# Optimization experiments

Hardware: AMD Instinct MI355X
Metric: run time of the kernel (lower is better)

## Reference

```python
import jax, jax.numpy as jnp
import numpy as np

B, H, L, D = 2, 16, 2048, 64


def setup_inputs() -> dict:
    key = jax.random.key(0)
    ks = jax.random.split(key, 5)
    q = jax.random.normal(ks[0], (B, H, L, D), dtype=jnp.float32)
    k = jax.random.normal(ks[1], (B, H, L, D), dtype=jnp.float32)
    v = jax.random.normal(ks[2], (B, H, L, D), dtype=jnp.float32)
    pe_q = jax.random.normal(ks[3], (B, H, L, D), dtype=jnp.float32)
    pe_k = jax.random.normal(ks[4], (B, H, L, D), dtype=jnp.float32)
    # causal mask, broadcast over batch: True = keep
    mask = jnp.broadcast_to(jnp.tril(jnp.ones((L, L), dtype=bool)), (B, L, L))
    return {"q": q, "k": k, "v": v, "pe_q": pe_q, "pe_k": pe_k, "mask": mask}


def reference(q, k, v, pe_q, pe_k, mask):
    scale = q.shape[-1] ** (-0.5)
    # dual-score: content QK^T + positional PE_Q PE_K^T, fused before softmax
    attn = (jnp.einsum('bhqd,bhkd->bhqk', q, k)
            + jnp.einsum('bhqd,bhkd->bhqk', pe_q, pe_k)) * scale
    # mask: [B, L, L] -> [B, 1, L, L]; False positions get -inf
    attn = jnp.where(mask[:, None, :, :], attn, -jnp.inf)
    attn = jax.nn.softmax(attn, axis=-1)
    return jnp.einsum('bhqk,bhkd->bhqd', attn, v)
```

## Files before the change

### kernel.cpp

```cpp
#include <hip/hip_runtime.h>
#include <hip/hip_bf16.h>


typedef unsigned short u16;
typedef unsigned int   u32;
typedef __attribute__((ext_vector_type(8))) short bf16x8;
typedef __attribute__((ext_vector_type(4))) float f32x4;

#define L_SEQ 2048
#define D_DIM 64
#define BQ    64
#define BK    32
#define NQT   (L_SEQ / BQ)

__device__ __forceinline__ float bf2f(u32 lo16) {
    u32 u = lo16 << 16; float f; __builtin_memcpy(&f, &u, 4); return f;
}

__device__ __forceinline__ u32 pack_hi16(u32 lo_src, u32 hi_src) {
    return __builtin_amdgcn_perm(hi_src, lo_src, 0x07060302u);
}

__global__ void detect_dtype_kernel(const u16* __restrict__ q, int* __restrict__ flag) {
    const int lane = threadIdx.x;
    float x = fabsf(bf2f((u32)q[lane]));
    bool big = !(x <= 100.f);
    unsigned long long m = __ballot(big);
    if (lane == 0) *flag = (m != 0ull) ? 1 : 0;
}

__device__ __forceinline__ void split_pack(const float* x, uint4& h, uint4& l) {
    u32 xb[8], rb[8];
#pragma unroll
    for (int j = 0; j < 8; ++j) {
        __builtin_memcpy(&xb[j], &x[j], 4);
        u32 hb = xb[j] & 0xffff0000u;
        float hf; __builtin_memcpy(&hf, &hb, 4);
        float r = x[j] - hf;
        __builtin_memcpy(&rb[j], &r, 4);
    }
    h.x = pack_hi16(xb[0], xb[1]);
    h.y = pack_hi16(xb[2], xb[3]);
    h.z = pack_hi16(xb[4], xb[5]);
    h.w = pack_hi16(xb[6], xb[7]);
    l.x = pack_hi16(rb[0], rb[1]);
    l.y = pack_hi16(rb[2], rb[3]);
    l.z = pack_hi16(rb[4], rb[5]);
    l.w = pack_hi16(rb[6], rb[7]);
}

template<bool IS_F32>
__device__ __forceinline__ void unpack8(const uint4& a, const uint4& b, float* x) {
    if (IS_F32) {
        u32 w[8] = {a.x, a.y, a.z, a.w, b.x, b.y, b.z, b.w};
#pragma unroll
        for (int j = 0; j < 8; ++j) __builtin_memcpy(&x[j], &w[j], 4);
    } else {
        u32 w[4] = {a.x, a.y, a.z, a.w};
#pragma unroll
        for (int j = 0; j < 4; ++j) {
            x[2*j]   = bf2f(w[j] & 0xffffu);
            x[2*j+1] = bf2f(w[j] >> 16);
        }
    }
}

struct StKE { uint4 k0, k1, e0, e1; };
struct StV  { u32 v[8]; };

template<bool IS_F32>
__device__ __forceinline__ void issue_ke(const void* Kv, const void* Ev,
        size_t base, int kbase, int r, int j8, StKE& R) {
    const size_t off = base + (size_t)(kbase + r) * D_DIM + j8 * 8;
    if (IS_F32) {
        const uint4* kp = (const uint4*)((const float*)Kv + off);
        R.k0 = kp[0]; R.k1 = kp[1];
        const uint4* ep = (const uint4*)((const float*)Ev + off);
        R.e0 = ep[0]; R.e1 = ep[1];
    } else {
        R.k0 = *(const uint4*)((const u16*)Kv + off);
        R.e0 = *(const uint4*)((const u16*)Ev + off);
    }
}

template<bool IS_F32>
__device__ __forceinline__ void issue_v(const void* Vv,
        size_t base, int kbase, int d, int kg, StV& R) {
    const size_t off = base + (size_t)(kbase + kg * 8) * D_DIM + d;
    if (IS_F32) {
        const u32* vp = (const u32*)((const float*)Vv + off);
#pragma unroll
        for (int j = 0; j < 8; ++j) R.v[j] = vp[j * D_DIM];
    } else {
        const u16* vp = (const u16*)Vv + off;
#pragma unroll
        for (int j = 0; j < 8; ++j) R.v[j] = (u32)vp[j * D_DIM];
    }
}

#define MFMA(a, b, c) __builtin_amdgcn_mfma_f32_16x16x32_bf16((a), (b), (c), 0, 0, 0)

template<bool IS_F32>
__global__ __launch_bounds__(512, 4) void attn_pair(
    const void* __restrict__ Qv, const void* __restrict__ Kv,
    const void* __restrict__ Vv, const void* __restrict__ PQv,
    const void* __restrict__ PKv, void* __restrict__ Ov,
    const int* __restrict__ flag)
{
    if (((*flag) != 0) != IS_F32) return;

    const int bh   = blockIdx.y;
    const int qa   = ((int)blockIdx.x + bh) & 15;
    const int t    = threadIdx.x;
    const int w    = t >> 6;
    const int lane = t & 63;
    const int g    = lane >> 4;
    const int c    = lane & 15;
    const size_t base = (size_t)bh * L_SEQ * D_DIM;
    const int qtile = (w < 4) ? qa : (31 - qa);
    const int qb_w  = qtile * BQ + (w & 3) * 16;
    const int nkt   = 64 - 2 * qa;

    __shared__ __align__(16) u16 Kt[2][BK * 128];
    __shared__ __align__(16) u16 Et[2][BK * 128];
    __shared__ __align__(16) u16 Vt[2][32 * 128];

    bf16x8 qa_h[4], qa_l[4];
    {
        const int qrow = qb_w + c;
#pragma unroll
        for (int ch = 0; ch < 4; ++ch) {
            const void* src = (ch < 2) ? Qv : PQv;
            const int d0 = (ch & 1) * 32 + 8 * g;
            const size_t off = base + (size_t)qrow * D_DIM + d0;
            float x[8];
            if (IS_F32) {
                const uint4* gp = (const uint4*)((const float*)src + off);
                unpack8<true>(gp[0], gp[1], x);
            } else {
                uint4 a = *(const uint4*)((const u16*)src + off);
                unpack8<false>(a, a, x);
            }
#pragma unroll
            for (int j = 0; j < 8; ++j) x[j] *= 0.1803368801f;
            uint4 hp, lp; split_pack(x, hp, lp);
            u32 hw[4] = {hp.x, hp.y, hp.z, hp.w}, lw[4] = {lp.x, lp.y, lp.z, lp.w};
#pragma unroll
            for (int j = 0; j < 4; ++j) {
                qa_h[ch][2*j]   = (short)(hw[j] & 0xffffu);
                qa_h[ch][2*j+1] = (short)(hw[j] >> 16);
                qa_l[ch][2*j]   = (short)(lw[j] & 0xffffu);
                qa_l[ch][2*j+1] = (short)(lw[j] >> 16);
            }
        }
    }

    float mr = -INFINITY, lr = 0.f;
    f32x4 acc[4];
#pragma unroll
    for (int df = 0; df < 4; ++df) acc[df] = (f32x4){0.f, 0.f, 0.f, 0.f};

    const bool is_ke = (t < 256);
    const int ts   = t & 255;
    const int r_t  = ts >> 3;
    const int j8_t = ts & 7;
    const int d_t  = ts & 63;
    const int kg_t = (ts >> 6) & 3;
    const int ke_wo = r_t * 128 + (j8_t ^ (r_t & 7)) * 8;
    const int v_rr  = d_t >> 1;
    const int v_wo  = v_rr * 128 + ((4 * (d_t & 1) + kg_t) ^ (v_rr & 7)) * 8;

    StKE Rke; StV Rv;

    auto stage_store = [&](int b) {
        if (is_ke) {
            float x[8]; uint4 hp, lp;
            unpack8<IS_F32>(Rke.k0, Rke.k1, x);
            split_pack(x, hp, lp);
            *(uint4*)(&Kt[b][0] + ke_wo)      = hp;
            *(uint4*)(&Kt[b][0] + ke_wo + 64) = lp;
            unpack8<IS_F32>(Rke.e0, Rke.e1, x);
            split_pack(x, hp, lp);
            *(uint4*)(&Et[b][0] + ke_wo)      = hp;
            *(uint4*)(&Et[b][0] + ke_wo + 64) = lp;
        } else {
            float x[8]; uint4 hp, lp;
#pragma unroll
            for (int j = 0; j < 8; ++j) {
                if (IS_F32) __builtin_memcpy(&x[j], &Rv.v[j], 4);
                else        x[j] = bf2f(Rv.v[j]);
            }
            split_pack(x, hp, lp);
            *(uint4*)(&Vt[b][0] + v_wo)      = hp;
            *(uint4*)(&Vt[b][0] + v_wo + 64) = lp;
        }
    };
    auto issue = [&](int kbase) {
        if (is_ke) issue_ke<IS_F32>(Kv, PKv, base, kbase, r_t, j8_t, Rke);
        else       issue_v <IS_F32>(Vv, base, kbase, d_t, kg_t, Rv);
    };

    issue(0);
    stage_store(0);
    issue(BK);
    __syncthreads();

    const int c7 = c & 7;
    const int srcA = 32 * (g & 1) + c;
    const int srcB = srcA + 16;
    const int sv = ((4 * (c & 1) + g) ^ ((c >> 1) & 7)) * 8;

    for (int kt = 0; kt < nkt; ++kt) {
        const int cur = kt & 1;
        const int kbase = kt * BK;
        const bool active = (kbase <= qb_w + 15);
        const bool do1 = (kbase + 16 <= qb_w + 15);

        f32x4 s0 = {0,0,0,0}, s1 = {0,0,0,0};
        if (active) {
            const u16* Ktc = &Kt[cur][0];
            const u16* Etc = &Et[cur][0];
            __builtin_amdgcn_s_setprio(1);
#pragma unroll
            for (int ch = 0; ch < 4; ++ch) {
                const u16* Bp = (ch < 2) ? Ktc : Etc;
                const int sh = ((((ch & 1) * 4 + g) ^ c7)) * 8;
                const u16* r0 = Bp + c * 128;
                bf16x8 b0h = *(const bf16x8*)(r0 + sh);
                bf16x8 b0l = *(const bf16x8*)(r0 + sh + 64);
                s0 = MFMA(b0h, qa_h[ch], s0);
                s0 = MFMA(b0l, qa_h[ch], s0);
                s0 = MFMA(b0h, qa_l[ch], s0);
                if (do1) {
                    const u16* r1 = Bp + (c + 16) * 128;
                    bf16x8 b1h = *(const bf16x8*)(r1 + sh);
                    bf16x8 b1l = *(const bf16x8*)(r1 + sh + 64);
                    s1 = MFMA(b1h, qa_h[ch], s1);
                    s1 = MFMA(b1l, qa_h[ch], s1);
                    s1 = MFMA(b1h, qa_l[ch], s1);
                }
            }
            __builtin_amdgcn_s_setprio(0);
        }

        if (kt + 1 < nkt) {
            stage_store(cur ^ 1);
            if (kt + 2 < nkt) issue(kbase + 2 * BK);
        }

        if (active) {
            const u16* Vtc = &Vt[cur][0];
            const int qrow = qb_w + c;
#pragma unroll
            for (int i = 0; i < 4; ++i) {
                if (kbase + 4 * g + i > qrow)                s0[i] = -INFINITY;
                if (!do1 || kbase + 16 + 4 * g + i > qrow)   s1[i] = -INFINITY;
            }
            float vm = fmaxf(fmaxf(fmaxf(s0[0], s0[1]), fmaxf(s0[2], s0[3])),
                             fmaxf(fmaxf(s1[0], s1[1]), fmaxf(s1[2], s1[3])));
            vm = fmaxf(vm, __shfl_xor(vm, 16));
            vm = fmaxf(vm, __shfl_xor(vm, 32));
            float p0f[4], p1f[4];
#pragma unroll
            for (int i = 0; i < 4; ++i) {
                p0f[i] = exp2f(s0[i] - mr);
                p1f[i] = exp2f(s1[i] - mr);
            }
            if (!__all(vm <= mr + 8.f)) {
                const float mn = fmaxf(mr, vm);
                const float al = exp2f(mr - mn);
                mr = mn;
                lr *= al;
                float al4[4];
#pragma unroll
                for (int i = 0; i < 4; ++i) al4[i] = __shfl(al, 20 * g + i);
#pragma unroll
                for (int df = 0; df < 4; ++df) {
#pragma unroll
                    for (int i = 0; i < 4; ++i) acc[df][i] *= al4[i];
                }
#pragma unroll
                for (int i = 0; i < 4; ++i) {
                    p0f[i] = exp2f(s0[i] - mr);
                    p1f[i] = exp2f(s1[i] - mr);
                }
            }
            float rs = (p0f[0] + p0f[1]) + (p0f[2] + p0f[3])
                     + (p1f[0] + p1f[1]) + (p1f[2] + p1f[3]);
            rs += __shfl_xor(rs, 16);
            rs += __shfl_xor(rs, 32);
            lr += rs;
            u32 w0[4], w1[4];
#pragma unroll
            for (int i = 0; i < 4; ++i) {
                const float x0 = p0f[i];
                u32 b0; __builtin_memcpy(&b0, &x0, 4);
                u32 h0 = b0 & 0xffff0000u; float h0f; __builtin_memcpy(&h0f, &h0, 4);
                float l0f = x0 - h0f; u32 l0; __builtin_memcpy(&l0, &l0f, 4);
                w0[i] = pack_hi16(b0, l0);
                const float x1 = p1f[i];
                u32 b1; __builtin_memcpy(&b1, &x1, 4);
                u32 h1 = b1 & 0xffff0000u; float h1f; __builtin_memcpy(&h1f, &h1, 4);
                float l1f = x1 - h1f; u32 l1; __builtin_memcpy(&l1, &l1f, 4);
                w1[i] = pack_hi16(b1, l1);
            }
            const bool lowhalf = (lane < 32);
            bf16x8 pa_h, pa_l;
#pragma unroll
            for (int i = 0; i < 4; ++i) {
                u32 t0a = (u32)__shfl((int)w0[i], srcA);
                u32 t1a = (u32)__shfl((int)w1[i], srcA);
                u32 t0b = (u32)__shfl((int)w0[i], srcB);
                u32 t1b = (u32)__shfl((int)w1[i], srcB);
                u32 ha = lowhalf ? t0a : t1a;
                u32 hb = lowhalf ? t0b : t1b;
                pa_h[i]     = (short)(ha & 0xffffu);
                pa_h[4 + i] = (short)(hb & 0xffffu);
                pa_l[i]     = (short)(ha >> 16);
                pa_l[4 + i] = (short)(hb >> 16);
            }
            __builtin_amdgcn_s_setprio(1);
#pragma unroll
            for (int df = 0; df < 4; ++df) {
                const u16* vw = Vtc + (8 * df + (c >> 1)) * 128;
                bf16x8 vbh = *(const bf16x8*)(vw + sv);
                bf16x8 vbl = *(const bf16x8*)(vw + sv + 64);
                acc[df] = MFMA(pa_h, vbh, acc[df]);
                acc[df] = MFMA(pa_h, vbl, acc[df]);
                acc[df] = MFMA(pa_l, vbh, acc[df]);
            }
            __builtin_amdgcn_s_setprio(0);
        }
        __syncthreads();
    }

    float inv[4];
#pragma unroll
    for (int i = 0; i < 4; ++i) inv[i] = 1.f / __shfl(lr, 20 * g + i);
    if (IS_F32) {
        float* o = (float*)Ov + base;
#pragma unroll
        for (int df = 0; df < 4; ++df)
#pragma unroll
            for (int i = 0; i < 4; ++i)
                o[(size_t)(qb_w + 4 * g + i) * D_DIM + 16 * df + c] = acc[df][i] * inv[i];
    } else {
        __hip_bfloat16* o = (__hip_bfloat16*)Ov + base;
#pragma unroll
        for (int df = 0; df < 4; ++df)
#pragma unroll
            for (int i = 0; i < 4; ++i)
                o[(size_t)(qb_w + 4 * g + i) * D_DIM + 16 * df + c] =
                    __float2bfloat16(acc[df][i] * inv[i]);
    }
}

extern "C" void kernel_launch(void* const* d_in, const int* in_sizes, int n_in,
                              void* d_out, int out_size, void* d_ws, size_t ws_size,
                              hipStream_t stream) {
    const void* q  = d_in[0];
    const void* k  = d_in[1];
    const void* v  = d_in[2];
    const void* pq = d_in[3];
    const void* pk = d_in[4];
    int* flag = (int*)d_ws;

    detect_dtype_kernel<<<1, 64, 0, stream>>>((const u16*)q, flag);

    dim3 grid(NQT / 2, 32);
    attn_pair<false><<<grid, 512, 0, stream>>>(q, k, v, pq, pk, d_out, flag);
    attn_pair<true ><<<grid, 512, 0, stream>>>(q, k, v, pq, pk, d_out, flag);
}
```

Baseline: 255.6 us.

## Split KV range across two 512-thread groups per block with LDS merge

```diff
diff --git a/kernel.cpp b/kernel.cpp
--- a/kernel.cpp
+++ b/kernel.cpp
@@ -101,7 +101,7 @@
 #define MFMA(a, b, c) __builtin_amdgcn_mfma_f32_16x16x32_bf16((a), (b), (c), 0, 0, 0)
 
 template<bool IS_F32>
-__global__ __launch_bounds__(512, 4) void attn_pair(
+__global__ __launch_bounds__(1024, 4) void attn_fused(
     const void* __restrict__ Qv, const void* __restrict__ Kv,
     const void* __restrict__ Vv, const void* __restrict__ PQv,
     const void* __restrict__ PKv, void* __restrict__ Ov,
@@ -109,59 +109,24 @@
 {
     if (((*flag) != 0) != IS_F32) return;
 
-    const int bh   = blockIdx.y;
-    const int qa   = ((int)blockIdx.x + bh) & 15;
-    const int t    = threadIdx.x;
-    const int w    = t >> 6;
+    const int bh  = blockIdx.y;
+    const int qp  = blockIdx.x;
+    const int t   = threadIdx.x;
+    const int grp = t >> 9;
+    const int tg  = t & 511;
+    const int w   = tg >> 6;
     const int lane = t & 63;
-    const int g    = lane >> 4;
-    const int c    = lane & 15;
+    const int g = lane >> 4, c = lane & 15;
     const size_t base = (size_t)bh * L_SEQ * D_DIM;
-    const int qtile = (w < 4) ? qa : (31 - qa);
-    const int qb_w  = qtile * BQ + (w & 3) * 16;
-    const int nkt   = 64 - 2 * qa;
-
-    __shared__ __align__(16) u16 Kt[2][BK * 128];
-    __shared__ __align__(16) u16 Et[2][BK * 128];
-    __shared__ __align__(16) u16 Vt[2][32 * 128];
-
-    bf16x8 qa_h[4], qa_l[4];
-    {
-        const int qrow = qb_w + c;
-#pragma unroll
-        for (int ch = 0; ch < 4; ++ch) {
-            const void* src = (ch < 2) ? Qv : PQv;
-            const int d0 = (ch & 1) * 32 + 8 * g;
-            const size_t off = base + (size_t)qrow * D_DIM + d0;
-            float x[8];
-            if (IS_F32) {
-                const uint4* gp = (const uint4*)((const float*)src + off);
-                unpack8<true>(gp[0], gp[1], x);
-            } else {
-                uint4 a = *(const uint4*)((const u16*)src + off);
-                unpack8<false>(a, a, x);
-            }
-#pragma unroll
-            for (int j = 0; j < 8; ++j) x[j] *= 0.1803368801f;
-            uint4 hp, lp; split_pack(x, hp, lp);
-            u32 hw[4] = {hp.x, hp.y, hp.z, hp.w}, lw[4] = {lp.x, lp.y, lp.z, lp.w};
-#pragma unroll
-            for (int j = 0; j < 4; ++j) {
-                qa_h[ch][2*j]   = (short)(hw[j] & 0xffffu);
-                qa_h[ch][2*j+1] = (short)(hw[j] >> 16);
-                qa_l[ch][2*j]   = (short)(lw[j] & 0xffffu);
-                qa_l[ch][2*j+1] = (short)(lw[j] >> 16);
-            }
-        }
-    }
-
-    float mr = -INFINITY, lr = 0.f;
-    f32x4 acc[4];
-#pragma unroll
-    for (int df = 0; df < 4; ++df) acc[df] = (f32x4){0.f, 0.f, 0.f, 0.f};
-
-    const bool is_ke = (t < 256);
-    const int ts   = t & 255;
+
+    __shared__ __align__(16) u16 Kt[2][2][BK * 128];
+    __shared__ __align__(16) u16 Et[2][2][BK * 128];
+    __shared__ __align__(16) u16 Vt[2][2][32 * 128];
+    __shared__ float Macc[8][16][64];
+    __shared__ float Mml[8][2][64];
+
+    const bool is_ke = (tg < 256);
+    const int ts   = tg & 255;
     const int r_t  = ts >> 3;
     const int j8_t = ts & 7;
     const int d_t  = ts & 63;
@@ -177,12 +142,12 @@
             float x[8]; uint4 hp, lp;
             unpack8<IS_F32>(Rke.k0, Rke.k1, x);
             split_pack(x, hp, lp);
-            *(uint4*)(&Kt[b][0] + ke_wo)      = hp;
-            *(uint4*)(&Kt[b][0] + ke_wo + 64) = lp;
+            *(uint4*)(&Kt[grp][b][0] + ke_wo)      = hp;
+            *(uint4*)(&Kt[grp][b][0] + ke_wo + 64) = lp;
             unpack8<IS_F32>(Rke.e0, Rke.e1, x);
             split_pack(x, hp, lp);
-            *(uint4*)(&Et[b][0] + ke_wo)      = hp;
-            *(uint4*)(&Et[b][0] + ke_wo + 64) = lp;
+            *(uint4*)(&Et[grp][b][0] + ke_wo)      = hp;
+            *(uint4*)(&Et[grp][b][0] + ke_wo + 64) = lp;
         } else {
             float x[8]; uint4 hp, lp;
 #pragma unroll
@@ -191,167 +156,238 @@
                 else        x[j] = bf2f(Rv.v[j]);
             }
             split_pack(x, hp, lp);
-            *(uint4*)(&Vt[b][0] + v_wo)      = hp;
-            *(uint4*)(&Vt[b][0] + v_wo + 64) = lp;
+            *(uint4*)(&Vt[grp][b][0] + v_wo)      = hp;
+            *(uint4*)(&Vt[grp][b][0] + v_wo + 64) = lp;
         }
     };
-    auto issue = [&](int kbase) {
-        if (is_ke) issue_ke<IS_F32>(Kv, PKv, base, kbase, r_t, j8_t, Rke);
-        else       issue_v <IS_F32>(Vv, base, kbase, d_t, kg_t, Rv);
+    auto issue = [&](int kb) {
+        if (is_ke) issue_ke<IS_F32>(Kv, PKv, base, kb, r_t, j8_t, Rke);
+        else       issue_v <IS_F32>(Vv, base, kb, d_t, kg_t, Rv);
     };
-
-    issue(0);
-    stage_store(0);
-    issue(BK);
-    __syncthreads();
 
     const int c7 = c & 7;
     const int srcA = 32 * (g & 1) + c;
     const int srcB = srcA + 16;
     const int sv = ((4 * (c & 1) + g) ^ ((c >> 1) & 7)) * 8;
 
-    for (int kt = 0; kt < nkt; ++kt) {
-        const int cur = kt & 1;
-        const int kbase = kt * BK;
-        const bool active = (kbase <= qb_w + 15);
-        const bool do1 = (kbase + 16 <= qb_w + 15);
-
-        f32x4 s0 = {0,0,0,0}, s1 = {0,0,0,0};
-        if (active) {
-            const u16* Ktc = &Kt[cur][0];
-            const u16* Etc = &Et[cur][0];
-            __builtin_amdgcn_s_setprio(1);
+    for (int seg = 0; seg < 2; ++seg) {
+        const int s    = seg ? (15 - qp) : qp;
+        const int half = 2 * s + 2;
+        const int k0   = grp ? half : 0;
+        const int klim = k0 + half;
+        const int qtile = 2 * s + ((w >= 4) ? 1 : 0);
+        const int qb_w  = qtile * BQ + (w & 3) * 16;
+
+        bf16x8 qa_h[4], qa_l[4];
+        {
+            const int qrow = qb_w + c;
 #pragma unroll
             for (int ch = 0; ch < 4; ++ch) {
-                const u16* Bp = (ch < 2) ? Ktc : Etc;
-                const int sh = ((((ch & 1) * 4 + g) ^ c7)) * 8;
-                const u16* r0 = Bp + c * 128;
-                bf16x8 b0h = *(const bf16x8*)(r0 + sh);
-                bf16x8 b0l = *(const bf16x8*)(r0 + sh + 64);
-                s0 = MFMA(b0h, qa_h[ch], s0);
-                s0 = MFMA(b0l, qa_h[ch], s0);
-                s0 = MFMA(b0h, qa_l[ch], s0);
-                if (do1) {
-                    const u16* r1 = Bp + (c + 16) * 128;
-                    bf16x8 b1h = *(const bf16x8*)(r1 + sh);
-                    bf16x8 b1l = *(const bf16x8*)(r1 + sh + 64);
-                    s1 = MFMA(b1h, qa_h[ch], s1);
-                    s1 = MFMA(b1l, qa_h[ch], s1);
-                    s1 = MFMA(b1h, qa_l[ch], s1);
-                }
-            }
-            __builtin_amdgcn_s_setprio(0);
-        }
-
-        if (kt + 1 < nkt) {
-            stage_store(cur ^ 1);
-            if (kt + 2 < nkt) issue(kbase + 2 * BK);
-        }
-
-        if (active) {
-            const u16* Vtc = &Vt[cur][0];
-            const int qrow = qb_w + c;
-#pragma unroll
-            for (int i = 0; i < 4; ++i) {
-                if (kbase + 4 * g + i > qrow)                s0[i] = -INFINITY;
-                if (!do1 || kbase + 16 + 4 * g + i > qrow)   s1[i] = -INFINITY;
-            }
-            float vm = fmaxf(fmaxf(fmaxf(s0[0], s0[1]), fmaxf(s0[2], s0[3])),
-                             fmaxf(fmaxf(s1[0], s1[1]), fmaxf(s1[2], s1[3])));
-            vm = fmaxf(vm, __shfl_xor(vm, 16));
-            vm = fmaxf(vm, __shfl_xor(vm, 32));
-            float p0f[4], p1f[4];
-#pragma unroll
-            for (int i = 0; i < 4; ++i) {
-                p0f[i] = exp2f(s0[i] - mr);
-                p1f[i] = exp2f(s1[i] - mr);
-            }
-            if (!__all(vm <= mr + 8.f)) {
-                const float mn = fmaxf(mr, vm);
-                const float al = exp2f(mr - mn);
-                mr = mn;
-                lr *= al;
-                float al4[4];
-#pragma unroll
-                for (int i = 0; i < 4; ++i) al4[i] = __shfl(al, 20 * g + i);
-#pragma unroll
-                for (int df = 0; df < 4; ++df) {
-#pragma unroll
-                    for (int i = 0; i < 4; ++i) acc[df][i] *= al4[i];
-                }
+                const void* src = (ch < 2) ? Qv : PQv;
+                const int d0 = (ch & 1) * 32 + 8 * g;
+                const size_t off = base + (size_t)qrow * D_DIM + d0;
+                float x[8];
+                if (IS_F32) {
+                    const uint4* gp = (const uint4*)((const float*)src + off);
+                    unpack8<true>(gp[0], gp[1], x);
+                } else {
+                    uint4 a = *(const uint4*)((const u16*)src + off);
+                    unpack8<false>(a, a, x);
+                }
+#pragma unroll
+                for (int j = 0; j < 8; ++j) x[j] *= 0.1803368801f;
+                uint4 hp, lp; split_pack(x, hp, lp);
+                u32 hw[4] = {hp.x, hp.y, hp.z, hp.w}, lw[4] = {lp.x, lp.y, lp.z, lp.w};
+#pragma unroll
+                for (int j = 0; j < 4; ++j) {
+                    qa_h[ch][2*j]   = (short)(hw[j] & 0xffffu);
+                    qa_h[ch][2*j+1] = (short)(hw[j] >> 16);
+                    qa_l[ch][2*j]   = (short)(lw[j] & 0xffffu);
+                    qa_l[ch][2*j+1] = (short)(lw[j] >> 16);
+                }
+            }
+        }
+
+        float mr = -INFINITY, lr = 0.f;
+        f32x4 acc[4];
+#pragma unroll
+        for (int df = 0; df < 4; ++df) acc[df] = (f32x4){0.f, 0.f, 0.f, 0.f};
+
+        issue(k0 * BK);
+        stage_store(0);
+        issue((k0 + 1) * BK);
+        __syncthreads();
+
+        for (int kt = k0; kt < klim; ++kt) {
+            const int cur = (kt - k0) & 1;
+            const int kbase = kt * BK;
+            const bool active = (kbase <= qb_w + 15);
+            const bool do1 = (kbase + 16 <= qb_w + 15);
+
+            f32x4 s0 = {0,0,0,0}, s1 = {0,0,0,0};
+            if (active) {
+                const u16* Ktc = &Kt[grp][cur][0];
+                const u16* Etc = &Et[grp][cur][0];
+                __builtin_amdgcn_s_setprio(1);
+#pragma unroll
+                for (int ch = 0; ch < 4; ++ch) {
+                    const u16* Bp = (ch < 2) ? Ktc : Etc;
+                    const int sh = ((((ch & 1) * 4 + g) ^ c7)) * 8;
+                    const u16* r0 = Bp + c * 128;
+                    bf16x8 b0h = *(const bf16x8*)(r0 + sh);
+                    bf16x8 b0l = *(const bf16x8*)(r0 + sh + 64);
+                    s0 = MFMA(b0h, qa_h[ch], s0);
+                    s0 = MFMA(b0l, qa_h[ch], s0);
+                    s0 = MFMA(b0h, qa_l[ch], s0);
+                    if (do1) {
+                        const u16* r1 = Bp + (c + 16) * 128;
+                        bf16x8 b1h = *(const bf16x8*)(r1 + sh);
+                        bf16x8 b1l = *(const bf16x8*)(r1 + sh + 64);
+                        s1 = MFMA(b1h, qa_h[ch], s1);
+                        s1 = MFMA(b1l, qa_h[ch], s1);
+                        s1 = MFMA(b1h, qa_l[ch], s1);
+                    }
+                }
+                __builtin_amdgcn_s_setprio(0);
+            }
+
+            if (kt + 1 < klim) {
+                stage_store(cur ^ 1);
+                if (kt + 2 < klim) issue((kt + 2) * BK);
+            }
+
+            if (active) {
+                const u16* Vtc = &Vt[grp][cur][0];
+                const int qrow = qb_w + c;
+#pragma unroll
+                for (int i = 0; i < 4; ++i) {
+                    if (kbase + 4 * g + i > qrow)                s0[i] = -INFINITY;
+                    if (!do1 || kbase + 16 + 4 * g + i > qrow)   s1[i] = -INFINITY;
+                }
+                float vm = fmaxf(fmaxf(fmaxf(s0[0], s0[1]), fmaxf(s0[2], s0[3])),
+                                 fmaxf(fmaxf(s1[0], s1[1]), fmaxf(s1[2], s1[3])));
+                vm = fmaxf(vm, __shfl_xor(vm, 16));
+                vm = fmaxf(vm, __shfl_xor(vm, 32));
+                float p0f[4], p1f[4];
 #pragma unroll
                 for (int i = 0; i < 4; ++i) {
                     p0f[i] = exp2f(s0[i] - mr);
                     p1f[i] = exp2f(s1[i] - mr);
                 }
-            }
-            float rs = (p0f[0] + p0f[1]) + (p0f[2] + p0f[3])
-                     + (p1f[0] + p1f[1]) + (p1f[2] + p1f[3]);
-            rs += __shfl_xor(rs, 16);
-            rs += __shfl_xor(rs, 32);
-            lr += rs;
-            u32 w0[4], w1[4];
+                if (!__all(vm <= mr + 8.f)) {
+                    const float mn = fmaxf(fmaxf(mr, vm), -1.0e30f);
+                    const float al = exp2f(mr - mn);
+                    mr = mn;
+                    lr *= al;
+                    float al4[4];
+#pragma unroll
+                    for (int i = 0; i < 4; ++i) al4[i] = __shfl(al, 20 * g + i);
+#pragma unroll
+                    for (int df = 0; df < 4; ++df) {
+#pragma unroll
+                        for (int i = 0; i < 4; ++i) acc[df][i] *= al4[i];
+                    }
+#pragma unroll
+                    for (int i = 0; i < 4; ++i) {
+                        p0f[i] = exp2f(s0[i] - mr);
+                        p1f[i] = exp2f(s1[i] - mr);
+                    }
+                }
+                float rs = (p0f[0] + p0f[1]) + (p0f[2] + p0f[3])
+                         + (p1f[0] + p1f[1]) + (p1f[2] + p1f[3]);
+                rs += __shfl_xor(rs, 16);
+                rs += __shfl_xor(rs, 32);
+                lr += rs;
+                u32 w0[4], w1[4];
+#pragma unroll
+                for (int i = 0; i < 4; ++i) {
+                    const float x0 = p0f[i];
+                    u32 b0; __builtin_memcpy(&b0, &x0, 4);
+                    u32 h0 = b0 & 0xffff0000u; float h0f; __builtin_memcpy(&h0f, &h0, 4);
+                    float l0f = x0 - h0f; u32 l0; __builtin_memcpy(&l0, &l0f, 4);
+                    w0[i] = pack_hi16(b0, l0);
+                    const float x1 = p1f[i];
+                    u32 b1; __builtin_memcpy(&b1, &x1, 4);
+                    u32 h1 = b1 & 0xffff0000u; float h1f; __builtin_memcpy(&h1f, &h1, 4);
+                    float l1f = x1 - h1f; u32 l1; __builtin_memcpy(&l1, &l1f, 4);
+                    w1[i] = pack_hi16(b1, l1);
+                }
+                const bool lowhalf = (lane < 32);
+                bf16x8 pa_h, pa_l;
+#pragma unroll
+                for (int i = 0; i < 4; ++i) {
+                    u32 t0a = (u32)__shfl((int)w0[i], srcA);
+                    u32 t1a = (u32)__shfl((int)w1[i], srcA);
+                    u32 t0b = (u32)__shfl((int)w0[i], srcB);
+                    u32 t1b = (u32)__shfl((int)w1[i], srcB);
+                    u32 ha = lowhalf ? t0a : t1a;
+                    u32 hb = lowhalf ? t0b : t1b;
+                    pa_h[i]     = (short)(ha & 0xffffu);
+                    pa_h[4 + i] = (short)(hb & 0xffffu);
+                    pa_l[i]     = (short)(ha >> 16);
+                    pa_l[4 + i] = (short)(hb >> 16);
+                }
+                __builtin_amdgcn_s_setprio(1);
+#pragma unroll
+                for (int df = 0; df < 4; ++df) {
+                    const u16* vw = Vtc + (8 * df + (c >> 1)) * 128;
+                    bf16x8 vbh = *(const bf16x8*)(vw + sv);
+                    bf16x8 vbl = *(const bf16x8*)(vw + sv + 64);
+                    acc[df] = MFMA(pa_h, vbh, acc[df]);
+                    acc[df] = MFMA(pa_h, vbl, acc[df]);
+                    acc[df] = MFMA(pa_l, vbh, acc[df]);
+                }
+                __builtin_amdgcn_s_setprio(0);
+            }
+            __syncthreads();
+        }
+
+        if (grp == 1) {
+            Mml[w][0][lane] = mr;
+            Mml[w][1][lane] = lr;
+#pragma unroll
+            for (int df = 0; df < 4; ++df)
+#pragma unroll
+                for (int i = 0; i < 4; ++i)
+                    Macc[w][df * 4 + i][lane] = acc[df][i];
+        }
+        __syncthreads();
+        if (grp == 0) {
+            const float m1 = Mml[w][0][lane];
+            const float l1 = Mml[w][1][lane];
+            const float m  = fmaxf(mr, m1);
+            const float wa = exp2f(mr - m);
+            const float wb = exp2f(m1 - m);
+            const float invl = 1.f / (lr * wa + l1 * wb);
+            float war[4], wbr[4], ir[4];
 #pragma unroll
             for (int i = 0; i < 4; ++i) {
-                const float x0 = p0f[i];
-                u32 b0; __builtin_memcpy(&b0, &x0, 4);
-                u32 h0 = b0 & 0xffff0000u; float h0f; __builtin_memcpy(&h0f, &h0, 4);
-                float l0f = x0 - h0f; u32 l0; __builtin_memcpy(&l0, &l0f, 4);
-                w0[i] = pack_hi16(b0, l0);
-                const float x1 = p1f[i];
-                u32 b1; __builtin_memcpy(&b1, &x1, 4);
-                u32 h1 = b1 & 0xffff0000u; float h1f; __builtin_memcpy(&h1f, &h1, 4);
-                float l1f = x1 - h1f; u32 l1; __builtin_memcpy(&l1, &l1f, 4);
-                w1[i] = pack_hi16(b1, l1);
-            }
-            const bool lowhalf = (lane < 32);
-            bf16x8 pa_h, pa_l;
-#pragma unroll
-            for (int i = 0; i < 4; ++i) {
-                u32 t0a = (u32)__shfl((int)w0[i], srcA);
-                u32 t1a = (u32)__shfl((int)w1[i], srcA);
-                u32 t0b = (u32)__shfl((int)w0[i], srcB);
-                u32 t1b = (u32)__shfl((int)w1[i], srcB);
-                u32 ha = lowhalf ? t0a : t1a;
-                u32 hb = lowhalf ? t0b : t1b;
-                pa_h[i]     = (short)(ha & 0xffffu);
-                pa_h[4 + i] = (short)(hb & 0xffffu);
-                pa_l[i]     = (short)(ha >> 16);
-                pa_l[4 + i] = (short)(hb >> 16);
-            }
-            __builtin_amdgcn_s_setprio(1);
-#pragma unroll
-            for (int df = 0; df < 4; ++df) {
-                const u16* vw = Vtc + (8 * df + (c >> 1)) * 128;
-                bf16x8 vbh = *(const bf16x8*)(vw + sv);
-                bf16x8 vbl = *(const bf16x8*)(vw + sv + 64);
-                acc[df] = MFMA(pa_h, vbh, acc[df]);
-                acc[df] = MFMA(pa_h, vbl, acc[df]);
-                acc[df] = MFMA(pa_l, vbh, acc[df]);
-            }
-            __builtin_amdgcn_s_setprio(0);
-        }
-        __syncthreads();
-    }
-
-    float inv[4];
-#pragma unroll
-    for (int i = 0; i < 4; ++i) inv[i] = 1.f / __shfl(lr, 20 * g + i);
-    if (IS_F32) {
-        float* o = (float*)Ov + base;
-#pragma unroll
-        for (int df = 0; df < 4; ++df)
-#pragma unroll
-            for (int i = 0; i < 4; ++i)
-                o[(size_t)(qb_w + 4 * g + i) * D_DIM + 16 * df + c] = acc[df][i] * inv[i];
-    } else {
-        __hip_bfloat16* o = (__hip_bfloat16*)Ov + base;
-#pragma unroll
-        for (int df = 0; df < 4; ++df)
-#pragma unroll
-            for (int i = 0; i < 4; ++i)
-                o[(size_t)(qb_w + 4 * g + i) * D_DIM + 16 * df + c] =
-                    __float2bfloat16(acc[df][i] * inv[i]);
+                war[i] = __shfl(wa,   20 * g + i);
+                wbr[i] = __shfl(wb,   20 * g + i);
+                ir[i]  = __shfl(invl, 20 * g + i);
+            }
+            if (IS_F32) {
+                float* o = (float*)Ov + base;
+#pragma unroll
+                for (int df = 0; df < 4; ++df)
+#pragma unroll
+                    for (int i = 0; i < 4; ++i) {
+                        const float ob = Macc[w][df * 4 + i][lane];
+                        o[(size_t)(qb_w + 4 * g + i) * D_DIM + 16 * df + c] =
+                            (acc[df][i] * war[i] + ob * wbr[i]) * ir[i];
+                    }
+            } else {
+                __hip_bfloat16* o = (__hip_bfloat16*)Ov + base;
+#pragma unroll
+                for (int df = 0; df < 4; ++df)
+#pragma unroll
+                    for (int i = 0; i < 4; ++i) {
+                        const float ob = Macc[w][df * 4 + i][lane];
+                        o[(size_t)(qb_w + 4 * g + i) * D_DIM + 16 * df + c] =
+                            __float2bfloat16((acc[df][i] * war[i] + ob * wbr[i]) * ir[i]);
+                    }
+            }
+        }
     }
 }
 
@@ -367,7 +403,7 @@
 
     detect_dtype_kernel<<<1, 64, 0, stream>>>((const u16*)q, flag);
 
-    dim3 grid(NQT / 2, 32);
-    attn_pair<false><<<grid, 512, 0, stream>>>(q, k, v, pq, pk, d_out, flag);
-    attn_pair<true ><<<grid, 512, 0, stream>>>(q, k, v, pq, pk, d_out, flag);
-}
+    dim3 grid(8, 32);
+    attn_fused<false><<<grid, 1024, 0, stream>>>(q, k, v, pq, pk, d_out, flag);
+    attn_fused<true ><<<grid, 1024, 0, stream>>>(q, k, v, pq, pk, d_out, flag);
+}
```

Measured after the change: 250.3 us. 2.1% less time.
